# Performance work log

Hardware: AMD Instinct MI355X
Metric: run time of the kernel (lower is better)

Reference implementation:

```python
import jax, jax.numpy as jnp
import numpy as np

B, N, C = 2, 8192, 64      # batch, points, feature channels
M = 2048                    # FPS-sampled centers (num_point)
KS = (16, 32)               # KNN sizes per scale
H, O = 128, 128             # EGNN hidden / output channels
S = len(KS)


def setup_inputs() -> dict:
    key = jax.random.key(0)
    k = jax.random.split(key, 12)
    sc = 0.05
    return {
        "points_xyz": jax.random.normal(k[0], (B, N, 3), jnp.float32),
        "features":   jax.random.normal(k[1], (B, C, N), jnp.float32),
        # edge MLP phi_e: [h_i, h_j, ||x_i-x_j||^2] -> H -> H
        "we1": jax.random.normal(k[2], (S, 2 * C + 1, H)) * sc,
        "be1": jnp.zeros((S, H)),
        "we2": jax.random.normal(k[3], (S, H, H)) * sc,
        "be2": jnp.zeros((S, H)),
        # coord MLP phi_x: H -> 1
        "wx": jax.random.normal(k[4], (S, H, 1)) * sc,
        "bx": jnp.zeros((S, 1)),
        # node MLP phi_h: [h_i, sum_j m_ij] -> H -> O
        "wh1": jax.random.normal(k[5], (S, C + H, H)) * sc,
        "bh1": jnp.zeros((S, H)),
        "wh2": jax.random.normal(k[6], (S, H, O)) * sc,
        "bh2": jnp.zeros((S, O)),
    }


def fps(xyz, m):
    """D-FPS: farthest point sampling by Euclidean distance. xyz (B,N,3) -> idx (B,m) int32."""
    b, n, _ = xyz.shape
    start = jnp.zeros((b,), jnp.int32)
    mind0 = jnp.full((b, n), 1e10, xyz.dtype)

    def step(carry, _):
        mind, last = carry
        lxyz = jnp.take_along_axis(xyz, last[:, None, None], axis=1)  # (B,1,3)
        d = jnp.sum((xyz - lxyz) ** 2, axis=-1)                       # (B,N)
        mind = jnp.minimum(mind, d)
        nxt = jnp.argmax(mind, axis=1).astype(jnp.int32)
        return (mind, nxt), nxt

    (_, _), rest = jax.lax.scan(step, (mind0, start), None, length=m - 1)
    return jnp.concatenate([start[:, None], rest.T], axis=1)  # (B,m)


def _forward(points_xyz, features, we1, be1, we2, be2, wx, bx, wh1, bh1, wh2, bh2):
    idx = fps(points_xyz, M)                                           # (B,M)
    dsamp_xyz = jnp.take_along_axis(points_xyz, idx[:, :, None], axis=1)   # (B,M,3)
    dsamp_feat = jnp.take_along_axis(features, idx[:, None, :], axis=2)    # (B,C,M)
    h_i = dsamp_feat.transpose(0, 2, 1)                                # (B,M,C)

    # pairwise squared distances centers->all points (B,M,N)
    d2 = (jnp.sum(dsamp_xyz ** 2, -1)[:, :, None]
          + jnp.sum(points_xyz ** 2, -1)[:, None, :]
          - 2.0 * jnp.einsum('bmd,bnd->bmn', dsamp_xyz, points_xyz))

    shifted, feats = [], []
    for i, k in enumerate(KS):
        _, nidx = jax.lax.top_k(-d2, k)                                # (B,M,k) KNN indices
        neigh_xyz = jax.vmap(lambda p, ii: p[ii])(points_xyz, nidx)    # (B,M,k,3)
        neigh_feat = jax.vmap(lambda f, ii: f[:, ii])(features, nidx)  # (B,C,M,k)
        h_j = neigh_feat.transpose(0, 2, 3, 1)                         # (B,M,k,C)

        rel = dsamp_xyz[:, :, None, :] - neigh_xyz                     # (B,M,k,3)
        dist2 = jnp.sum(rel * rel, -1, keepdims=True)                  # (B,M,k,1)

        e_in = jnp.concatenate(
            [jnp.broadcast_to(h_i[:, :, None, :], h_j.shape), h_j, dist2], axis=-1)
        m_ij = jax.nn.silu(e_in @ we1[i] + be1[i])
        m_ij = jax.nn.silu(m_ij @ we2[i] + be2[i])                     # (B,M,k,H)

        coef = m_ij @ wx[i] + bx[i]                                    # (B,M,k,1)
        x_shift = dsamp_xyz + jnp.mean(rel * coef, axis=2)             # (B,M,3)

        agg = jnp.sum(m_ij, axis=2)                                    # (B,M,H)
        h_out = jax.nn.silu(jnp.concatenate([h_i, agg], -1) @ wh1[i] + bh1[i]) @ wh2[i] + bh2[i]

        shifted.append(x_shift)
        feats.append(h_out.transpose(0, 2, 1))                         # (B,O,M)

    return (dsamp_xyz,
            jnp.concatenate(shifted, axis=1),    # (B, S*M, 3)
            jnp.concatenate(feats, axis=1),      # (B, S*O, M)
            idx)


def reference(points_xyz, features, we1, be1, we2, be2, wx, bx, wh1, bh1, wh2, bh2):
    return _forward(points_xyz, features, we1, be1, we2, be2, wx, bx, wh1, bh1, wh2, bh2)
```

## Files before the change

### kernel.cpp

```cpp
#include <hip/hip_runtime.h>
#include <stdint.h>
#include <math.h>

#define NPTS  8192
#define NB    2
#define NC    64
#define MCENT 2048
#define HH    128
#define K2NN  32

#define OUT0_OFF 0
#define OUT1_OFF (NB*MCENT*3)
#define OUT2_OFF (OUT1_OFF + NB*2*MCENT*3)
#define OUT3_OFF (OUT2_OFF + NB*2*HH*MCENT)

__device__ __forceinline__ float silu_f(float v){ return v / (1.0f + expf(-v)); }

template<int CTRL>
__device__ __forceinline__ unsigned dppk(unsigned v){
  return (unsigned)__builtin_amdgcn_update_dpp((int)v, (int)v, CTRL, 0xF, 0xF, false);
}
__device__ __forceinline__ unsigned wave_max_u32_sgpr(unsigned v){
  unsigned s;
  s = dppk<0xB1>(v);  v = v > s ? v : s;
  s = dppk<0x4E>(v);  v = v > s ? v : s;
  s = dppk<0x141>(v); v = v > s ? v : s;
  s = dppk<0x140>(v); v = v > s ? v : s;
  s = dppk<0x142>(v); v = v > s ? v : s;
  s = dppk<0x143>(v); v = v > s ? v : s;
  return (unsigned)__builtin_amdgcn_readlane((int)v, 63);
}
__device__ __forceinline__ unsigned wave_min_u32_sgpr(unsigned v){
  unsigned s;
  s = dppk<0xB1>(v);  v = v < s ? v : s;
  s = dppk<0x4E>(v);  v = v < s ? v : s;
  s = dppk<0x141>(v); v = v < s ? v : s;
  s = dppk<0x140>(v); v = v < s ? v : s;
  s = dppk<0x142>(v); v = v < s ? v : s;
  s = dppk<0x143>(v); v = v < s ? v : s;
  return (unsigned)__builtin_amdgcn_readlane((int)v, 63);
}

__device__ __forceinline__ void bar_lds(){
  asm volatile("s_waitcnt lgkmcnt(0)" ::: "memory");
  __builtin_amdgcn_s_barrier();
  __builtin_amdgcn_sched_barrier(0);
}

__global__ __launch_bounds__(256, 2) void fps_kernel(const float* __restrict__ xyz,
                                                     float* __restrict__ out,
                                                     int* __restrict__ ws_idx){
#pragma clang fp contract(off)
  __shared__ float xs[NPTS], ys[NPTS], zs[NPTS];
  __shared__ unsigned long long warr[2][4];
  const int b    = blockIdx.x;
  const int tid  = threadIdx.x;
  const int lane = tid & 63, wid = tid >> 6;
  const float* P = xyz + (size_t)b * NPTS * 3;

  float x[32], y[32], z[32], mind[32];
  #pragma unroll
  for (int j = 0; j < 32; ++j){
    const int p = tid*32 + j;
    const float px = P[p*3+0], py = P[p*3+1], pz = P[p*3+2];
    x[j] = px; y[j] = py; z[j] = pz; mind[j] = 1e10f;
    xs[p] = px; ys[p] = py; zs[p] = pz;
  }
  float cx = P[0], cy = P[1], cz = P[2];
  if (tid == 0){
    ws_idx[b*MCENT] = 0;
    out[OUT3_OFF + b*MCENT] = 0.0f;
    out[OUT0_OFF + (size_t)(b*MCENT)*3 + 0] = cx;
    out[OUT0_OFF + (size_t)(b*MCENT)*3 + 1] = cy;
    out[OUT0_OFF + (size_t)(b*MCENT)*3 + 2] = cz;
  }
  __syncthreads();

  for (int t = 1; t < MCENT; ++t){
    float bestv = -1.0f; int bestp = tid*32;
    #pragma unroll
    for (int j = 0; j < 32; ++j){
      const float dx = x[j]-cx, dy = y[j]-cy, dz = z[j]-cz;
      const float d  = (dx*dx + dy*dy) + dz*dz;
      const float mn = fminf(mind[j], d);
      mind[j] = mn;
      if (mn > bestv){ bestv = mn; bestp = tid*32 + j; }
    }
    const unsigned vb = __float_as_uint(bestv);
    const unsigned wv = wave_max_u32_sgpr(vb);
    const unsigned long long bal = __ballot(vb == wv);
    const int wl = __ffsll(bal) - 1;
    const int wp = __builtin_amdgcn_readlane(bestp, wl);
    if (lane == 0)
      warr[t & 1][wid] = ((unsigned long long)wv << 32) | (unsigned)(NPTS-1-wp);
    bar_lds();
    unsigned long long kb = warr[t & 1][0];
    #pragma unroll
    for (int w = 1; w < 4; ++w){
      const unsigned long long k2 = warr[t & 1][w];
      if (k2 > kb) kb = k2;
    }
    const int p = NPTS - 1 - (int)(kb & 0xFFFFFFFFULL);
    cx = xs[p]; cy = ys[p]; cz = zs[p];
    if (tid == 0){
      ws_idx[b*MCENT + t] = p;
      out[OUT3_OFF + b*MCENT + t] = (float)p;
      out[OUT0_OFF + (size_t)(b*MCENT + t)*3 + 0] = cx;
      out[OUT0_OFF + (size_t)(b*MCENT + t)*3 + 1] = cy;
      out[OUT0_OFF + (size_t)(b*MCENT + t)*3 + 2] = cz;
    }
  }
}

#define S1STR 132
#define C_D2U   0
#define C_S1    0
#define C_S2    16896
#define C_HJ    33792
#define C_HI    41984
#define C_REL   42240
#define C_D2S   42624
#define C_AGG   42752
#define C_T1    43264
#define C_COEF  43776
#define C_NIDX  43904
#define C_WARR  44032
#define C_SIZE  44096

template<int KNB>
__device__ __forceinline__ void egnn_scale(
    int isc, int b, int m, int tid,
    const float* __restrict__ we1, const float* __restrict__ be1,
    const float* __restrict__ we2, const float* __restrict__ be2,
    const float* __restrict__ wxw, const float* __restrict__ bxw,
    const float* __restrict__ wh1, const float* __restrict__ bh1,
    const float* __restrict__ wh2, const float* __restrict__ bh2,
    const float* hi, const float (*hj)[NC], const float (*rel)[3],
    const float* d2s, float (*s1)[S1STR], float (*s2)[S1STR],
    float* coefs, float* aggs, float* t1,
    float cx, float cy, float cz, float* __restrict__ out)
{
  constexpr int KH = KNB/2;
  const int h  = tid & 127;
  const int jg = tid >> 7;
  const int j0 = jg * KH;
  const float* W1 = we1 + (size_t)isc*129*HH;
  const float* W2 = we2 + (size_t)isc*HH*HH;

  float shi = be1[isc*HH + h];
  for (int r = 0; r < NC; ++r) shi += hi[r] * W1[r*HH + h];
  float acc[KH];
  #pragma unroll
  for (int jl = 0; jl < KH; ++jl) acc[jl] = shi;
  for (int r4 = 0; r4 < NC/4; ++r4){
    const float w0 = W1[(NC + 4*r4+0)*HH + h];
    const float w1 = W1[(NC + 4*r4+1)*HH + h];
    const float w2 = W1[(NC + 4*r4+2)*HH + h];
    const float w3 = W1[(NC + 4*r4+3)*HH + h];
    #pragma unroll
    for (int jl = 0; jl < KH; ++jl){
      const float4 v = *(const float4*)&hj[j0+jl][4*r4];
      acc[jl] += v.x*w0; acc[jl] += v.y*w1; acc[jl] += v.z*w2; acc[jl] += v.w*w3;
    }
  }
  {
    const float wd = W1[128*HH + h];
    #pragma unroll
    for (int jl = 0; jl < KH; ++jl)
      s1[j0+jl][h] = silu_f(acc[jl] + d2s[j0+jl]*wd);
  }
  __syncthreads();

  float acc2[KH];
  {
    const float b2 = be2[isc*HH + h];
    #pragma unroll
    for (int jl = 0; jl < KH; ++jl) acc2[jl] = b2;
  }
  for (int r4 = 0; r4 < HH/4; ++r4){
    const float w0 = W2[(4*r4+0)*HH + h];
    const float w1 = W2[(4*r4+1)*HH + h];
    const float w2 = W2[(4*r4+2)*HH + h];
    const float w3 = W2[(4*r4+3)*HH + h];
    #pragma unroll
    for (int jl = 0; jl < KH; ++jl){
      const float4 v = *(const float4*)&s1[j0+jl][4*r4];
      acc2[jl] += v.x*w0; acc2[jl] += v.y*w1; acc2[jl] += v.z*w2; acc2[jl] += v.w*w3;
    }
  }
  #pragma unroll
  for (int jl = 0; jl < KH; ++jl)
    s2[j0+jl][h] = silu_f(acc2[jl]);
  __syncthreads();

  if (tid < HH){
    float a = 0.f;
    #pragma unroll
    for (int j = 0; j < KNB; ++j) a += s2[j][tid];
    aggs[tid] = a;
  } else if (tid < HH + KNB){
    const int j = tid - HH;
    const float* WX = wxw + isc*HH;
    float c = 0.f;
    for (int r = 0; r < HH; ++r) c += s2[j][r]*WX[r];
    coefs[j] = c + bxw[isc];
  }
  __syncthreads();

  if (tid < 3){
    float s = 0.f;
    #pragma unroll
    for (int j = 0; j < KNB; ++j) s += rel[j][tid]*coefs[j];
    const float cc = (tid==0) ? cx : ((tid==1) ? cy : cz);
    out[OUT1_OFF + ((size_t)(b*2 + isc)*MCENT + m)*3 + tid] = cc + s*(1.0f/KNB);
  }

  if (tid < HH){
    const float* WH1 = wh1 + (size_t)isc*(NC+HH)*HH;
    float n = bh1[isc*HH + tid];
    for (int r = 0; r < NC; ++r) n += hi[r]*WH1[r*HH + tid];
    for (int r = 0; r < HH; ++r) n += aggs[r]*WH1[(NC+r)*HH + tid];
    t1[tid] = silu_f(n);
  }
  __syncthreads();

  if (tid < HH){
    const float* WH2 = wh2 + (size_t)isc*HH*HH;
    float v = bh2[isc*HH + tid];
    for (int r = 0; r < HH; ++r) v += t1[r]*WH2[r*HH + tid];
    out[OUT2_OFF + ((size_t)(b*2*HH) + isc*HH + tid)*MCENT + m] = v;
  }
  __syncthreads();
}

__global__ __launch_bounds__(256) void knn_egnn_kernel(
    const float* __restrict__ xyz,  const float* __restrict__ feat,
    const float* __restrict__ we1,  const float* __restrict__ be1,
    const float* __restrict__ we2,  const float* __restrict__ be2,
    const float* __restrict__ wxw,  const float* __restrict__ bxw,
    const float* __restrict__ wh1,  const float* __restrict__ bh1,
    const float* __restrict__ wh2,  const float* __restrict__ bh2,
    const int* __restrict__ ws_idx, float* __restrict__ out)
{
#pragma clang fp contract(off)
  __shared__ __align__(16) char smem[C_SIZE];
  unsigned* d2u = (unsigned*)(smem + C_D2U);
  float (*s1)[S1STR] = (float (*)[S1STR])(smem + C_S1);
  float (*s2)[S1STR] = (float (*)[S1STR])(smem + C_S2);
  float (*hj)[NC]    = (float (*)[NC])(smem + C_HJ);
  float* hi    = (float*)(smem + C_HI);
  float (*rel)[3] = (float (*)[3])(smem + C_REL);
  float* d2s   = (float*)(smem + C_D2S);
  float* aggs  = (float*)(smem + C_AGG);
  float* t1    = (float*)(smem + C_T1);
  float* coefs = (float*)(smem + C_COEF);
  int*   nidx  = (int*)(smem + C_NIDX);
  unsigned long long (*warr)[4] = (unsigned long long (*)[4])(smem + C_WARR);

  const int blk = blockIdx.x;
  const int b = blk / MCENT, m = blk % MCENT;
  const int tid = threadIdx.x;
  const float* P = xyz + (size_t)b*NPTS*3;
  const float cx = out[OUT0_OFF + (size_t)(b*MCENT+m)*3 + 0];
  const float cy = out[OUT0_OFF + (size_t)(b*MCENT+m)*3 + 1];
  const float cz = out[OUT0_OFF + (size_t)(b*MCENT+m)*3 + 2];

  {
    const float cn = (cx*cx + cy*cy) + cz*cz;
    unsigned long long best = ~0ULL, second = ~0ULL;
    #pragma unroll 4
    for (int j = 0; j < NPTS/256; ++j){
      const int p = tid + 256*j;
      const float px = P[p*3+0], py = P[p*3+1], pz = P[p*3+2];
      const float pn = (px*px + py*py) + pz*pz;
      const float e  = (cx*px + cy*py) + cz*pz;
      const float d2 = (cn + pn) - 2.0f*e;
      unsigned u = __float_as_uint(d2);
      u = (u & 0x80000000u) ? ~u : (u | 0x80000000u);
      d2u[p] = u;
      const unsigned long long kk = ((unsigned long long)u << 32) | (unsigned)p;
      if      (kk < best)  { second = best; best = kk; }
      else if (kk < second){ second = kk; }
    }
    __syncthreads();

    for (int it = 0; it < K2NN; ++it){
      const unsigned vb = (unsigned)(best >> 32);
      const unsigned wv = wave_min_u32_sgpr(vb);
      const unsigned long long bal = __ballot(vb == wv);
      unsigned long long k;
      if (__popcll(bal) == 1){
        const int wl = __ffsll(bal) - 1;
        const unsigned lp = (unsigned)__builtin_amdgcn_readlane((int)(unsigned)best, wl);
        k = ((unsigned long long)wv << 32) | lp;
      } else {
        k = best;
        #pragma unroll
        for (int o = 32; o > 0; o >>= 1){
          const unsigned long long k2 = __shfl_xor(k, o);
          if (k2 < k) k = k2;
        }
      }
      if ((tid & 63) == 0) warr[it & 1][tid >> 6] = k;
      __syncthreads();
      unsigned long long kb = warr[it & 1][0];
      #pragma unroll
      for (int w = 1; w < 4; ++w){
        const unsigned long long k2 = warr[it & 1][w];
        if (k2 < kb) kb = k2;
      }
      const unsigned p = (unsigned)kb;
      if (tid == 0) nidx[it] = (int)p;
      if (best == kb){
        d2u[p] = 0xFFFFFFFFu;
        best = second; second = ~0ULL;
        if (best == ~0ULL){
          #pragma unroll 4
          for (int j = 0; j < NPTS/256; ++j){
            const int q = tid + 256*j;
            const unsigned long long kk = ((unsigned long long)d2u[q] << 32) | (unsigned)q;
            if      (kk < best)  { second = best; best = kk; }
            else if (kk < second){ second = kk; }
          }
        }
      }
    }
    __syncthreads();
  }

  const int ci = ws_idx[b*MCENT + m];
  if (tid < NC) hi[tid] = feat[((size_t)b*NC + tid)*NPTS + ci];
  if (tid < K2NN){
    const int p = nidx[tid];
    const float rx = cx - P[p*3+0];
    const float ry = cy - P[p*3+1];
    const float rz = cz - P[p*3+2];
    rel[tid][0]=rx; rel[tid][1]=ry; rel[tid][2]=rz;
    d2s[tid] = rx*rx + ry*ry + rz*rz;
  }
  {
    const int j  = tid >> 3;
    const int c0 = (tid & 7) * 8;
    const int p  = nidx[j];
    #pragma unroll
    for (int q = 0; q < 8; ++q)
      hj[j][c0+q] = feat[((size_t)b*NC + c0 + q)*NPTS + p];
  }
  __syncthreads();

  egnn_scale<16>(0, b, m, tid, we1, be1, we2, be2, wxw, bxw, wh1, bh1, wh2, bh2,
                 hi, hj, rel, d2s, s1, s2, coefs, aggs, t1, cx, cy, cz, out);
  egnn_scale<32>(1, b, m, tid, we1, be1, we2, be2, wxw, bxw, wh1, bh1, wh2, bh2,
                 hi, hj, rel, d2s, s1, s2, coefs, aggs, t1, cx, cy, cz, out);
}

extern "C" void kernel_launch(void* const* d_in, const int* in_sizes, int n_in,
                              void* d_out, int out_size, void* d_ws, size_t ws_size,
                              hipStream_t stream){
  const float* xyz = (const float*)d_in[0];
  const float* feat= (const float*)d_in[1];
  const float* we1 = (const float*)d_in[2];
  const float* be1 = (const float*)d_in[3];
  const float* we2 = (const float*)d_in[4];
  const float* be2 = (const float*)d_in[5];
  const float* wxw = (const float*)d_in[6];
  const float* bxw = (const float*)d_in[7];
  const float* wh1 = (const float*)d_in[8];
  const float* bh1 = (const float*)d_in[9];
  const float* wh2 = (const float*)d_in[10];
  const float* bh2 = (const float*)d_in[11];
  float* out = (float*)d_out;

  int* ws_idx = (int*)d_ws;

  fps_kernel     <<<dim3(NB),       dim3(256), 0, stream>>>(xyz, out, ws_idx);
  knn_egnn_kernel<<<dim3(NB*MCENT), dim3(256), 0, stream>>>(xyz, feat,
      we1, be1, we2, be2, wxw, bxw, wh1, bh1, wh2, bh2, ws_idx, out);
}
```

Baseline: 2.301 ms.

## Fuse FPS and KNN/EGNN into persistent producer-consumer kernel with work queue

Merges the serial FPS kernel and the per-center KNN+EGNN kernel into one persistent launch. Two blocks run FPS and publish each sampled index to a global flag array. The remaining blocks pull work items through an atomic counter and spin until their center's index is published, so neighbor search and the MLPs overlap with the long sequential FPS loop. Consumer blocks on the same CU as an FPS block exit so they do not slow the producers. The cost is added spin-wait and atomic traffic, relaxed-ordering memory risks, and a reliance on all blocks being co-resident.

```diff
diff --git a/kernel.cpp b/kernel.cpp
--- a/kernel.cpp
+++ b/kernel.cpp
@@ -8,109 +8,19 @@
 #define MCENT 2048
 #define HH    128
 #define K2NN  32
+#define NITEMS (NB*MCENT)
+#define SENT  0xFFFFFFFFu
+#define GRID  764
 
 #define OUT0_OFF 0
 #define OUT1_OFF (NB*MCENT*3)
 #define OUT2_OFF (OUT1_OFF + NB*2*MCENT*3)
 #define OUT3_OFF (OUT2_OFF + NB*2*HH*MCENT)
 
-__device__ __forceinline__ float silu_f(float v){ return v / (1.0f + expf(-v)); }
-
-template<int CTRL>
-__device__ __forceinline__ unsigned dppk(unsigned v){
-  return (unsigned)__builtin_amdgcn_update_dpp((int)v, (int)v, CTRL, 0xF, 0xF, false);
-}
-__device__ __forceinline__ unsigned wave_max_u32_sgpr(unsigned v){
-  unsigned s;
-  s = dppk<0xB1>(v);  v = v > s ? v : s;
-  s = dppk<0x4E>(v);  v = v > s ? v : s;
-  s = dppk<0x141>(v); v = v > s ? v : s;
-  s = dppk<0x140>(v); v = v > s ? v : s;
-  s = dppk<0x142>(v); v = v > s ? v : s;
-  s = dppk<0x143>(v); v = v > s ? v : s;
-  return (unsigned)__builtin_amdgcn_readlane((int)v, 63);
-}
-__device__ __forceinline__ unsigned wave_min_u32_sgpr(unsigned v){
-  unsigned s;
-  s = dppk<0xB1>(v);  v = v < s ? v : s;
-  s = dppk<0x4E>(v);  v = v < s ? v : s;
-  s = dppk<0x141>(v); v = v < s ? v : s;
-  s = dppk<0x140>(v); v = v < s ? v : s;
-  s = dppk<0x142>(v); v = v < s ? v : s;
-  s = dppk<0x143>(v); v = v < s ? v : s;
-  return (unsigned)__builtin_amdgcn_readlane((int)v, 63);
-}
-
-__device__ __forceinline__ void bar_lds(){
-  asm volatile("s_waitcnt lgkmcnt(0)" ::: "memory");
-  __builtin_amdgcn_s_barrier();
-  __builtin_amdgcn_sched_barrier(0);
-}
-
-__global__ __launch_bounds__(256, 2) void fps_kernel(const float* __restrict__ xyz,
-                                                     float* __restrict__ out,
-                                                     int* __restrict__ ws_idx){
-#pragma clang fp contract(off)
-  __shared__ float xs[NPTS], ys[NPTS], zs[NPTS];
-  __shared__ unsigned long long warr[2][4];
-  const int b    = blockIdx.x;
-  const int tid  = threadIdx.x;
-  const int lane = tid & 63, wid = tid >> 6;
-  const float* P = xyz + (size_t)b * NPTS * 3;
-
-  float x[32], y[32], z[32], mind[32];
-  #pragma unroll
-  for (int j = 0; j < 32; ++j){
-    const int p = tid*32 + j;
-    const float px = P[p*3+0], py = P[p*3+1], pz = P[p*3+2];
-    x[j] = px; y[j] = py; z[j] = pz; mind[j] = 1e10f;
-    xs[p] = px; ys[p] = py; zs[p] = pz;
-  }
-  float cx = P[0], cy = P[1], cz = P[2];
-  if (tid == 0){
-    ws_idx[b*MCENT] = 0;
-    out[OUT3_OFF + b*MCENT] = 0.0f;
-    out[OUT0_OFF + (size_t)(b*MCENT)*3 + 0] = cx;
-    out[OUT0_OFF + (size_t)(b*MCENT)*3 + 1] = cy;
-    out[OUT0_OFF + (size_t)(b*MCENT)*3 + 2] = cz;
-  }
-  __syncthreads();
-
-  for (int t = 1; t < MCENT; ++t){
-    float bestv = -1.0f; int bestp = tid*32;
-    #pragma unroll
-    for (int j = 0; j < 32; ++j){
-      const float dx = x[j]-cx, dy = y[j]-cy, dz = z[j]-cz;
-      const float d  = (dx*dx + dy*dy) + dz*dz;
-      const float mn = fminf(mind[j], d);
-      mind[j] = mn;
-      if (mn > bestv){ bestv = mn; bestp = tid*32 + j; }
-    }
-    const unsigned vb = __float_as_uint(bestv);
-    const unsigned wv = wave_max_u32_sgpr(vb);
-    const unsigned long long bal = __ballot(vb == wv);
-    const int wl = __ffsll(bal) - 1;
-    const int wp = __builtin_amdgcn_readlane(bestp, wl);
-    if (lane == 0)
-      warr[t & 1][wid] = ((unsigned long long)wv << 32) | (unsigned)(NPTS-1-wp);
-    bar_lds();
-    unsigned long long kb = warr[t & 1][0];
-    #pragma unroll
-    for (int w = 1; w < 4; ++w){
-      const unsigned long long k2 = warr[t & 1][w];
-      if (k2 > kb) kb = k2;
-    }
-    const int p = NPTS - 1 - (int)(kb & 0xFFFFFFFFULL);
-    cx = xs[p]; cy = ys[p]; cz = zs[p];
-    if (tid == 0){
-      ws_idx[b*MCENT + t] = p;
-      out[OUT3_OFF + b*MCENT + t] = (float)p;
-      out[OUT0_OFF + (size_t)(b*MCENT + t)*3 + 0] = cx;
-      out[OUT0_OFF + (size_t)(b*MCENT + t)*3 + 1] = cy;
-      out[OUT0_OFF + (size_t)(b*MCENT + t)*3 + 2] = cz;
-    }
-  }
-}
+#define W_PA    0
+#define W_FCU0  4096
+#define W_FCU1  4097
+#define W_NEXT  4098
 
 #define S1STR 132
 #define C_D2U   0
@@ -125,7 +35,104 @@
 #define C_COEF  43776
 #define C_NIDX  43904
 #define C_WARR  44032
-#define C_SIZE  44096
+#define C_PB    44096
+#define C_SIZE  44160
+
+__device__ __forceinline__ float silu_f(float v){ return v / (1.0f + expf(-v)); }
+
+template<int CTRL>
+__device__ __forceinline__ unsigned dppk(unsigned v){
+  return (unsigned)__builtin_amdgcn_update_dpp((int)v, (int)v, CTRL, 0xF, 0xF, false);
+}
+__device__ __forceinline__ unsigned wave_max_u32_sgpr(unsigned v){
+  unsigned s;
+  s = dppk<0xB1>(v);  v = v > s ? v : s;
+  s = dppk<0x4E>(v);  v = v > s ? v : s;
+  s = dppk<0x141>(v); v = v > s ? v : s;
+  s = dppk<0x140>(v); v = v > s ? v : s;
+  s = dppk<0x142>(v); v = v > s ? v : s;
+  s = dppk<0x143>(v); v = v > s ? v : s;
+  return (unsigned)__builtin_amdgcn_readlane((int)v, 63);
+}
+__device__ __forceinline__ unsigned wave_min_u32_sgpr(unsigned v){
+  unsigned s;
+  s = dppk<0xB1>(v);  v = v < s ? v : s;
+  s = dppk<0x4E>(v);  v = v < s ? v : s;
+  s = dppk<0x141>(v); v = v < s ? v : s;
+  s = dppk<0x140>(v); v = v < s ? v : s;
+  s = dppk<0x142>(v); v = v < s ? v : s;
+  s = dppk<0x143>(v); v = v < s ? v : s;
+  return (unsigned)__builtin_amdgcn_readlane((int)v, 63);
+}
+
+__device__ __forceinline__ void bar_lds(){
+  asm volatile("s_waitcnt lgkmcnt(0)" ::: "memory");
+  __builtin_amdgcn_s_barrier();
+  __builtin_amdgcn_sched_barrier(0);
+}
+
+__device__ __forceinline__ unsigned cu_sig(){
+  unsigned hwid, xcc;
+  asm volatile("s_getreg_b32 %0, hwreg(4, 8, 8)" : "=s"(hwid));
+  asm volatile("s_getreg_b32 %0, hwreg(HW_REG_XCC_ID)" : "=s"(xcc));
+  return (xcc << 8) | (hwid & 0xFFu);
+}
+
+__device__ void fps_role(const int b, const int tid,
+                         const float* __restrict__ xyz,
+                         unsigned* __restrict__ ws, char* smem)
+{
+#pragma clang fp contract(off)
+  unsigned long long (*warr)[4] = (unsigned long long (*)[4])(smem + C_WARR);
+  const int lane = tid & 63, wid = tid >> 6;
+  const float* P = xyz + (size_t)b * NPTS * 3;
+
+  if (tid == 0){
+    __hip_atomic_store(&ws[W_FCU0 + b], cu_sig(), __ATOMIC_RELAXED, __HIP_MEMORY_SCOPE_AGENT);
+    __hip_atomic_store(&ws[W_PA + (0<<1) + b], 0u, __ATOMIC_RELAXED, __HIP_MEMORY_SCOPE_AGENT);
+  }
+
+  float x[32], y[32], z[32], mind[32];
+  #pragma unroll
+  for (int j = 0; j < 32; ++j){
+    const int p = tid*32 + j;
+    x[j] = P[p*3+0]; y[j] = P[p*3+1]; z[j] = P[p*3+2];
+    mind[j] = 1e10f;
+  }
+  float cx = P[0], cy = P[1], cz = P[2];
+  __syncthreads();
+
+  for (int t = 1; t < MCENT; ++t){
+    float bestv = -1.0f; int bestp = tid*32;
+    #pragma unroll
+    for (int j = 0; j < 32; ++j){
+      const float dx = x[j]-cx, dy = y[j]-cy, dz = z[j]-cz;
+      const float d  = (dx*dx + dy*dy) + dz*dz;
+      const float mn = fminf(mind[j], d);
+      mind[j] = mn;
+      if (mn > bestv){ bestv = mn; bestp = tid*32 + j; }
+    }
+    const unsigned vb = __float_as_uint(bestv);
+    const unsigned wv = wave_max_u32_sgpr(vb);
+    const unsigned long long bal = __ballot(vb == wv);
+    const int wl = __ffsll(bal) - 1;
+    const int wp = __builtin_amdgcn_readlane(bestp, wl);
+    if (lane == 0)
+      warr[t & 1][wid] = ((unsigned long long)wv << 32) | (unsigned)(NPTS-1-wp);
+    bar_lds();
+    unsigned long long kb = warr[t & 1][0];
+    #pragma unroll
+    for (int w = 1; w < 4; ++w){
+      const unsigned long long k2 = warr[t & 1][w];
+      if (k2 > kb) kb = k2;
+    }
+    const int p = NPTS - 1 - (int)(kb & 0xFFFFFFFFULL);
+    cx = P[p*3+0]; cy = P[p*3+1]; cz = P[p*3+2];
+    if (tid == 0)
+      __hip_atomic_store(&ws[W_PA + (t<<1) + b], (unsigned)p,
+                         __ATOMIC_RELAXED, __HIP_MEMORY_SCOPE_AGENT);
+  }
+}
 
 template<int KNB>
 __device__ __forceinline__ void egnn_scale(
@@ -214,7 +221,6 @@
     const float cc = (tid==0) ? cx : ((tid==1) ? cy : cz);
     out[OUT1_OFF + ((size_t)(b*2 + isc)*MCENT + m)*3 + tid] = cc + s*(1.0f/KNB);
   }
-
   if (tid < HH){
     const float* WH1 = wh1 + (size_t)isc*(NC+HH)*HH;
     float n = bh1[isc*HH + tid];
@@ -223,7 +229,6 @@
     t1[tid] = silu_f(n);
   }
   __syncthreads();
-
   if (tid < HH){
     const float* WH2 = wh2 + (size_t)isc*HH*HH;
     float v = bh2[isc*HH + tid];
@@ -233,17 +238,16 @@
   __syncthreads();
 }
 
-__global__ __launch_bounds__(256) void knn_egnn_kernel(
-    const float* __restrict__ xyz,  const float* __restrict__ feat,
-    const float* __restrict__ we1,  const float* __restrict__ be1,
-    const float* __restrict__ we2,  const float* __restrict__ be2,
-    const float* __restrict__ wxw,  const float* __restrict__ bxw,
-    const float* __restrict__ wh1,  const float* __restrict__ bh1,
-    const float* __restrict__ wh2,  const float* __restrict__ bh2,
-    const int* __restrict__ ws_idx, float* __restrict__ out)
+__device__ void consumer_role(const int tid,
+    const float* __restrict__ xyz, const float* __restrict__ feat,
+    const float* __restrict__ we1, const float* __restrict__ be1,
+    const float* __restrict__ we2, const float* __restrict__ be2,
+    const float* __restrict__ wxw, const float* __restrict__ bxw,
+    const float* __restrict__ wh1, const float* __restrict__ bh1,
+    const float* __restrict__ wh2, const float* __restrict__ bh2,
+    unsigned* __restrict__ ws, float* __restrict__ out, char* smem)
 {
 #pragma clang fp contract(off)
-  __shared__ __align__(16) char smem[C_SIZE];
   unsigned* d2u = (unsigned*)(smem + C_D2U);
   float (*s1)[S1STR] = (float (*)[S1STR])(smem + C_S1);
   float (*s2)[S1STR] = (float (*)[S1STR])(smem + C_S2);
@@ -256,102 +260,162 @@
   float* coefs = (float*)(smem + C_COEF);
   int*   nidx  = (int*)(smem + C_NIDX);
   unsigned long long (*warr)[4] = (unsigned long long (*)[4])(smem + C_WARR);
-
-  const int blk = blockIdx.x;
-  const int b = blk / MCENT, m = blk % MCENT;
-  const int tid = threadIdx.x;
-  const float* P = xyz + (size_t)b*NPTS*3;
-  const float cx = out[OUT0_OFF + (size_t)(b*MCENT+m)*3 + 0];
-  const float cy = out[OUT0_OFF + (size_t)(b*MCENT+m)*3 + 1];
-  const float cz = out[OUT0_OFF + (size_t)(b*MCENT+m)*3 + 2];
-
-  {
-    const float cn = (cx*cx + cy*cy) + cz*cz;
-    unsigned long long best = ~0ULL, second = ~0ULL;
-    #pragma unroll 4
-    for (int j = 0; j < NPTS/256; ++j){
-      const int p = tid + 256*j;
-      const float px = P[p*3+0], py = P[p*3+1], pz = P[p*3+2];
-      const float pn = (px*px + py*py) + pz*pz;
-      const float e  = (cx*px + cy*py) + cz*pz;
-      const float d2 = (cn + pn) - 2.0f*e;
-      unsigned u = __float_as_uint(d2);
-      u = (u & 0x80000000u) ? ~u : (u | 0x80000000u);
-      d2u[p] = u;
-      const unsigned long long kk = ((unsigned long long)u << 32) | (unsigned)p;
-      if      (kk < best)  { second = best; best = kk; }
-      else if (kk < second){ second = kk; }
+  int*   pb    = (int*)(smem + C_PB);
+
+  if (tid == 0){
+    unsigned f0 = SENT, f1 = SENT; long n = 0;
+    for (;;){
+      f0 = __hip_atomic_load(&ws[W_FCU0], __ATOMIC_RELAXED, __HIP_MEMORY_SCOPE_AGENT);
+      f1 = __hip_atomic_load(&ws[W_FCU1], __ATOMIC_RELAXED, __HIP_MEMORY_SCOPE_AGENT);
+      if (f0 != SENT && f1 != SENT) break;
+      __builtin_amdgcn_s_sleep(8);
+      if (++n > 1000000L) break;
+    }
+    const unsigned sig = cu_sig();
+    pb[2] = (sig == f0 || sig == f1) ? 1 : 0;
+  }
+  __syncthreads();
+  if (pb[2]) return;
+
+  for (;;){
+    if (tid == 0){
+      const unsigned i = atomicAdd(&ws[W_NEXT], 1u);
+      pb[0] = (int)i;
+      if (i < NITEMS){
+        unsigned pv = __hip_atomic_load(&ws[W_PA + i], __ATOMIC_RELAXED, __HIP_MEMORY_SCOPE_AGENT);
+        long n = 0;
+        while (pv == SENT){
+          __builtin_amdgcn_s_sleep(16);
+          pv = __hip_atomic_load(&ws[W_PA + i], __ATOMIC_RELAXED, __HIP_MEMORY_SCOPE_AGENT);
+          if (++n > 3000000L) break;
+        }
+        pb[1] = (pv >= NPTS) ? 0 : (int)pv;
+      }
     }
     __syncthreads();
-
-    for (int it = 0; it < K2NN; ++it){
-      const unsigned vb = (unsigned)(best >> 32);
-      const unsigned wv = wave_min_u32_sgpr(vb);
-      const unsigned long long bal = __ballot(vb == wv);
-      unsigned long long k;
-      if (__popcll(bal) == 1){
-        const int wl = __ffsll(bal) - 1;
-        const unsigned lp = (unsigned)__builtin_amdgcn_readlane((int)(unsigned)best, wl);
-        k = ((unsigned long long)wv << 32) | lp;
-      } else {
-        k = best;
+    const int item = pb[0];
+    if (item >= NITEMS) return;
+    const int p = pb[1];
+    const int m = item >> 1, b = item & 1;
+    const float* P = xyz + (size_t)b*NPTS*3;
+    const float cx = P[p*3+0], cy = P[p*3+1], cz = P[p*3+2];
+    if (tid == 0) out[OUT3_OFF + b*MCENT + m] = (float)p;
+    if (tid < 3)  out[OUT0_OFF + (size_t)(b*MCENT+m)*3 + tid] = P[p*3+tid];
+
+    {
+      const float cn = (cx*cx + cy*cy) + cz*cz;
+      unsigned long long best = ~0ULL, second = ~0ULL;
+      #pragma unroll 4
+      for (int j = 0; j < NPTS/256; ++j){
+        const int q = tid + 256*j;
+        const float px = P[q*3+0], py = P[q*3+1], pz = P[q*3+2];
+        const float pn = (px*px + py*py) + pz*pz;
+        const float e  = (cx*px + cy*py) + cz*pz;
+        const float d2 = (cn + pn) - 2.0f*e;
+        unsigned u = __float_as_uint(d2);
+        u = (u & 0x80000000u) ? ~u : (u | 0x80000000u);
+        d2u[q] = u;
+        const unsigned long long kk = ((unsigned long long)u << 32) | (unsigned)q;
+        if      (kk < best)  { second = best; best = kk; }
+        else if (kk < second){ second = kk; }
+      }
+      __syncthreads();
+
+      for (int it = 0; it < K2NN; ++it){
+        const unsigned vb = (unsigned)(best >> 32);
+        const unsigned wv = wave_min_u32_sgpr(vb);
+        const unsigned long long bal = __ballot(vb == wv);
+        unsigned long long k;
+        if (__popcll(bal) == 1){
+          const int wl = __ffsll(bal) - 1;
+          const unsigned lp = (unsigned)__builtin_amdgcn_readlane((int)(unsigned)best, wl);
+          k = ((unsigned long long)wv << 32) | lp;
+        } else {
+          k = best;
+          #pragma unroll
+          for (int o = 32; o > 0; o >>= 1){
+            const unsigned long long k2 = __shfl_xor(k, o);
+            if (k2 < k) k = k2;
+          }
+        }
+        if ((tid & 63) == 0) warr[it & 1][tid >> 6] = k;
+        __syncthreads();
+        unsigned long long kb = warr[it & 1][0];
         #pragma unroll
-        for (int o = 32; o > 0; o >>= 1){
-          const unsigned long long k2 = __shfl_xor(k, o);
-          if (k2 < k) k = k2;
+        for (int w = 1; w < 4; ++w){
+          const unsigned long long k2 = warr[it & 1][w];
+          if (k2 < kb) kb = k2;
         }
-      }
-      if ((tid & 63) == 0) warr[it & 1][tid >> 6] = k;
-      __syncthreads();
-      unsigned long long kb = warr[it & 1][0];
-      #pragma unroll
-      for (int w = 1; w < 4; ++w){
-        const unsigned long long k2 = warr[it & 1][w];
-        if (k2 < kb) kb = k2;
-      }
-      const unsigned p = (unsigned)kb;
-      if (tid == 0) nidx[it] = (int)p;
-      if (best == kb){
-        d2u[p] = 0xFFFFFFFFu;
-        best = second; second = ~0ULL;
-        if (best == ~0ULL){
-          #pragma unroll 4
-          for (int j = 0; j < NPTS/256; ++j){
-            const int q = tid + 256*j;
-            const unsigned long long kk = ((unsigned long long)d2u[q] << 32) | (unsigned)q;
-            if      (kk < best)  { second = best; best = kk; }
-            else if (kk < second){ second = kk; }
+        const unsigned q = (unsigned)kb;
+        if (tid == 0) nidx[it] = (int)q;
+        if (best == kb){
+          d2u[q] = 0xFFFFFFFFu;
+          best = second; second = ~0ULL;
+          if (best == ~0ULL){
+            #pragma unroll 4
+            for (int j = 0; j < NPTS/256; ++j){
+              const int r = tid + 256*j;
+              const unsigned long long kk = ((unsigned long long)d2u[r] << 32) | (unsigned)r;
+              if      (kk < best)  { second = best; best = kk; }
+              else if (kk < second){ second = kk; }
+            }
           }
         }
       }
+      __syncthreads();
+    }
+
+    if (tid < NC) hi[tid] = feat[((size_t)b*NC + tid)*NPTS + p];
+    if (tid < K2NN){
+      const int q = nidx[tid];
+      const float rx = cx - P[q*3+0];
+      const float ry = cy - P[q*3+1];
+      const float rz = cz - P[q*3+2];
+      rel[tid][0]=rx; rel[tid][1]=ry; rel[tid][2]=rz;
+      d2s[tid] = rx*rx + ry*ry + rz*rz;
+    }
+    {
+      const int j  = tid >> 3;
+      const int c0 = (tid & 7) * 8;
+      const int q  = nidx[j];
+      #pragma unroll
+      for (int w = 0; w < 8; ++w)
+        hj[j][c0+w] = feat[((size_t)b*NC + c0 + w)*NPTS + q];
     }
     __syncthreads();
-  }
-
-  const int ci = ws_idx[b*MCENT + m];
-  if (tid < NC) hi[tid] = feat[((size_t)b*NC + tid)*NPTS + ci];
-  if (tid < K2NN){
-    const int p = nidx[tid];
-    const float rx = cx - P[p*3+0];
-    const float ry = cy - P[p*3+1];
-    const float rz = cz - P[p*3+2];
-    rel[tid][0]=rx; rel[tid][1]=ry; rel[tid][2]=rz;
-    d2s[tid] = rx*rx + ry*ry + rz*rz;
-  }
-  {
-    const int j  = tid >> 3;
-    const int c0 = (tid & 7) * 8;
-    const int p  = nidx[j];
-    #pragma unroll
-    for (int q = 0; q < 8; ++q)
-      hj[j][c0+q] = feat[((size_t)b*NC + c0 + q)*NPTS + p];
-  }
-  __syncthreads();
-
-  egnn_scale<16>(0, b, m, tid, we1, be1, we2, be2, wxw, bxw, wh1, bh1, wh2, bh2,
-                 hi, hj, rel, d2s, s1, s2, coefs, aggs, t1, cx, cy, cz, out);
-  egnn_scale<32>(1, b, m, tid, we1, be1, we2, be2, wxw, bxw, wh1, bh1, wh2, bh2,
-                 hi, hj, rel, d2s, s1, s2, coefs, aggs, t1, cx, cy, cz, out);
+
+    egnn_scale<16>(0, b, m, tid, we1, be1, we2, be2, wxw, bxw, wh1, bh1, wh2, bh2,
+                   hi, hj, rel, d2s, s1, s2, coefs, aggs, t1, cx, cy, cz, out);
+    egnn_scale<32>(1, b, m, tid, we1, be1, we2, be2, wxw, bxw, wh1, bh1, wh2, bh2,
+                   hi, hj, rel, d2s, s1, s2, coefs, aggs, t1, cx, cy, cz, out);
+  }
+}
+
+__global__ __launch_bounds__(256, 3) void fused_kernel(
+    const float* __restrict__ xyz, const float* __restrict__ feat,
+    const float* __restrict__ we1, const float* __restrict__ be1,
+    const float* __restrict__ we2, const float* __restrict__ be2,
+    const float* __restrict__ wxw, const float* __restrict__ bxw,
+    const float* __restrict__ wh1, const float* __restrict__ bh1,
+    const float* __restrict__ wh2, const float* __restrict__ bh2,
+    unsigned* __restrict__ ws, float* __restrict__ out)
+{
+  __shared__ __align__(16) char smem[C_SIZE];
+  const int tid = threadIdx.x;
+  if (blockIdx.x < NB){
+    fps_role((int)blockIdx.x, tid, xyz, ws, smem);
+  } else {
+    consumer_role(tid, xyz, feat, we1,be1,we2,be2,wxw,bxw,wh1,bh1,wh2,bh2,
+                  ws, out, smem);
+  }
+}
+
+__global__ void init_kernel(unsigned* __restrict__ ws){
+  const int i = threadIdx.x + blockIdx.x * blockDim.x;
+  if (i < NITEMS)            ws[W_PA + i] = SENT;
+  else if (i == NITEMS)      ws[W_FCU0] = SENT;
+  else if (i == NITEMS + 1)  ws[W_FCU1] = SENT;
+  else if (i == NITEMS + 2)  ws[W_NEXT] = 0;
 }
 
 extern "C" void kernel_launch(void* const* d_in, const int* in_sizes, int n_in,
@@ -371,9 +435,9 @@
   const float* bh2 = (const float*)d_in[11];
   float* out = (float*)d_out;
 
-  int* ws_idx = (int*)d_ws;
-
-  fps_kernel     <<<dim3(NB),       dim3(256), 0, stream>>>(xyz, out, ws_idx);
-  knn_egnn_kernel<<<dim3(NB*MCENT), dim3(256), 0, stream>>>(xyz, feat,
-      we1, be1, we2, be2, wxw, bxw, wh1, bh1, wh2, bh2, ws_idx, out);
-}
+  unsigned* ws = (unsigned*)d_ws;
+
+  init_kernel <<<dim3(5),    dim3(1024), 0, stream>>>(ws);
+  fused_kernel<<<dim3(GRID), dim3(256),  0, stream>>>(xyz, feat,
+      we1, be1, we2, be2, wxw, bxw, wh1, bh1, wh2, bh2, ws, out);
+}
```

Result: slower. 2.505 ms (+8.9%).
